# Kernel optimization log

Hardware: AMD Instinct MI355X
Metric: run time of the kernel (lower is better)

## Reference

```python
import jax, jax.numpy as jnp
import numpy as np

T, B, F_, H, D, C = 16, 1024, 512, 128, 8, 100  # trees, batch, feat, hidden, depth, classes
L = 2 ** (D + 1)  # n_leaf = 512


def _routing_tables():
    # Static per-leaf routing: node index and branch side at each depth.
    # Derived from compute_mu's gather indices:
    #   node(d, l) = 2^d - 1 + l // 2^(D+1-d);  side(d, l) = (l // 2^(D-d)) % 2
    l = np.arange(L)
    node = np.stack([(2 ** d - 1) + l // (2 ** (D + 1 - d)) for d in range(D + 1)])  # [D+1, L]
    side = np.stack([(l // (2 ** (D - d))) % 2 for d in range(D + 1)])               # [D+1, L]
    return jnp.asarray(node, dtype=jnp.int32), jnp.asarray(side.astype(np.bool_))


def setup_inputs() -> dict:
    key = jax.random.key(0)
    ks = jax.random.split(key, 4)
    return {
        "feat": jax.random.normal(ks[0], (B, F_), jnp.float32),
        "W1": jax.random.normal(ks[1], (T, F_, H), jnp.float32) * 0.05,
        "b1": jnp.zeros((T, H), jnp.float32),
        "W2": jax.random.normal(ks[2], (T, H, L), jnp.float32) * 0.05,
        "b2": jnp.zeros((T, L), jnp.float32),
        "pi": jax.random.uniform(ks[3], (T, L, C), jnp.float32, -2.0, 2.0),
    }


def reference(feat, W1, b1, W2, b2, pi):
    node, side = _routing_tables()
    # Per-tree MLP head (dropout is identity in eval mode).
    h = jax.nn.relu(jnp.einsum('bf,tfh->tbh', feat, W1) + b1[:, None, :])        # [T,B,H]
    p = jax.nn.sigmoid(jnp.einsum('tbh,thl->tbl', h, W2) + b2[:, None, :])       # [T,B,L]
    # compute_mu: product of routing probs along each root->leaf path.
    sel = p[:, :, node]                          # [T,B,D+1,L] gather (static indices)
    route = jnp.where(side, 1.0 - sel, sel)      # left -> p, right -> 1-p
    mu = jnp.prod(route, axis=2)                 # [T,B,L]
    # compute_py_x: mean over leaves then mean over trees of mu @ softmax(pi).
    leaf_p = jax.nn.softmax(pi, axis=-1)         # [T,L,C]
    py_x = jnp.einsum('tbl,tlc->bc', mu, leaf_p) / (L * T)  # [B,C]
    return jnp.log(py_x)
```

## Files before the change

kernel.cpp:

```cpp
#include <hip/hip_runtime.h>
#include <hip/hip_bf16.h>
#include <math.h>

#define T_ 16
#define B_ 1024
#define F_ 512
#define H_ 128
#define D_ 8
#define C_ 100
#define L_ 512
#define CP_ 112

typedef __attribute__((ext_vector_type(8))) short bf16x8_t;
typedef __attribute__((ext_vector_type(4))) float f32x4_t;

__device__ inline ushort f2bf(float x) {
  __hip_bfloat16 b = __float2bfloat16(x);
  return *(ushort*)&b;
}
__device__ inline float bf2f(ushort u) {
  union { unsigned int i; float f; } v;
  v.i = ((unsigned int)u) << 16;
  return v.f;
}

__global__ __launch_bounds__(256) void k_prep(
    const float* __restrict__ feat, const float* __restrict__ W1,
    const float* __restrict__ W2, const float* __restrict__ pi,
    ushort* __restrict__ feat_bf, ushort* __restrict__ W1T,
    ushort* __restrict__ W2T, ushort* __restrict__ lpT) {
  __shared__ ushort ubuf[112 * 48];
  float (*tile)[33] = (float(*)[33])ubuf;
  ushort (*tileT)[48] = (ushort(*)[48])ubuf;
  const int bid = blockIdx.x, tid = threadIdx.x;

  if (bid < 256) {
    int i = (bid * 256 + tid) * 8;
    float4 a = *(const float4*)(feat + i);
    float4 b = *(const float4*)(feat + i + 4);
    bf16x8_t o;
    o[0] = (short)f2bf(a.x); o[1] = (short)f2bf(a.y);
    o[2] = (short)f2bf(a.z); o[3] = (short)f2bf(a.w);
    o[4] = (short)f2bf(b.x); o[5] = (short)f2bf(b.y);
    o[6] = (short)f2bf(b.z); o[7] = (short)f2bf(b.w);
    *(bf16x8_t*)(feat_bf + i) = o;
    return;
  }
  if (bid < 2304) {
    const float* X; ushort* XT; int K, N, kb, nb, s;
    if (bid < 1280) {
      int r = bid - 256;  kb = r & 15; nb = (r >> 4) & 3;  s = r >> 6;
      X = W1; XT = W1T; K = F_; N = H_;
    } else {
      int r = bid - 1280; kb = r & 3;  nb = (r >> 2) & 15; s = r >> 6;
      X = W2; XT = W2T; K = H_; N = L_;
    }
    const int k0 = kb * 32, n0 = nb * 32;
    const int c = tid & 31, r0 = tid >> 5;
    const float* Xs = X + (size_t)s * K * N;
    ushort* XTs = XT + (size_t)s * N * K;
#pragma unroll
    for (int j = 0; j < 4; ++j)
      tile[r0 + 8 * j][c] = Xs[(size_t)(k0 + r0 + 8 * j) * N + n0 + c];
    __syncthreads();
#pragma unroll
    for (int j = 0; j < 4; ++j)
      XTs[(size_t)(n0 + r0 + 8 * j) * K + k0 + c] = f2bf(tile[c][r0 + 8 * j]);
    return;
  }
  {
    int bid2 = bid - 2304;
    int t = bid2 >> 4, l0 = (bid2 & 15) << 5;
    int lane = tid & 63;
#pragma unroll
    for (int p = 0; p < 8; ++p) {
      int rl = p * 4 + (tid >> 6);
      const float* x = pi + (size_t)(t * L_ + l0 + rl) * C_;
      float v0 = (lane < C_) ? x[lane] : -1e30f;
      float v1 = (lane + 64 < C_) ? x[lane + 64] : -1e30f;
      float m = fmaxf(v0, v1);
#pragma unroll
      for (int off = 32; off; off >>= 1) m = fmaxf(m, __shfl_xor(m, off, 64));
      float e0 = __expf(v0 - m);
      float e1 = (lane + 64 < C_) ? __expf(v1 - m) : 0.0f;
      float sm = e0 + e1;
#pragma unroll
      for (int off = 32; off; off >>= 1) sm += __shfl_xor(sm, off, 64);
      float inv = 1.0f / sm;
      if (lane < C_) tileT[lane][rl] = f2bf(e0 * inv);
      int c2 = lane + 64;
      if (c2 < CP_) tileT[c2][rl] = f2bf(c2 < C_ ? e1 * inv : 0.0f);
    }
    __syncthreads();
    ushort* dst = lpT + (size_t)t * CP_ * L_ + l0;
    for (int idx = tid; idx < 448; idx += 256) {
      int c = idx >> 2, ch = (idx & 3) * 8;
      *(bf16x8_t*)(dst + (size_t)c * L_ + ch) = *(const bf16x8_t*)&tileT[c][ch];
    }
  }
}

__global__ __launch_bounds__(256) void k12_mfma(
    const ushort* __restrict__ feat, const ushort* __restrict__ W1T,
    const float* __restrict__ b1, const ushort* __restrict__ W2T,
    const float* __restrict__ b2, const ushort* __restrict__ lpT,
    float* __restrict__ part) {
  __shared__ ushort smem[29696];
  ushort (*h_s)[136] = (ushort(*)[136])smem;
  ushort (*a_s)[72]  = (ushort(*)[72])(smem + 4352);
  ushort (*b_s)[72]  = (ushort(*)[72])(smem + 6656);
  ushort (*w_s)[136] = (ushort(*)[136])(smem + 4352);
  ushort (*p_s)[520] = (ushort(*)[520])(smem + 13056);

  const int bid = blockIdx.x;
  const int t = bid & 15, b0 = (bid >> 4) * 32;
  const int tid = threadIdx.x;
  const int w = tid >> 6, lane = tid & 63, quad = lane >> 4, n = lane & 15;

  const int arow = tid >> 3, acol = (tid & 7) * 8;
  const ushort* featp = feat + (size_t)(b0 + arow) * F_ + acol;
  const ushort* w1p   = W1T + ((size_t)t * H_ + arow) * F_ + acol;

  {
    f32x4_t acc[2][2];
#pragma unroll
    for (int i = 0; i < 2; ++i)
#pragma unroll
      for (int j = 0; j < 2; ++j) acc[i][j] = (f32x4_t){0.f, 0.f, 0.f, 0.f};

    bf16x8_t ra, rb[4];
    ra = *(const bf16x8_t*)(featp);
#pragma unroll
    for (int i = 0; i < 4; ++i)
      rb[i] = *(const bf16x8_t*)(w1p + (size_t)i * 32 * F_);
    *(bf16x8_t*)&a_s[arow][acol] = ra;
#pragma unroll
    for (int i = 0; i < 4; ++i)
      *(bf16x8_t*)&b_s[i * 32 + arow][acol] = rb[i];
    __syncthreads();
    ra = *(const bf16x8_t*)(featp + 64);
#pragma unroll
    for (int i = 0; i < 4; ++i)
      rb[i] = *(const bf16x8_t*)(w1p + (size_t)i * 32 * F_ + 64);

#pragma unroll
    for (int kc = 0; kc < 8; ++kc) {
#pragma unroll
      for (int ks = 0; ks < 64; ks += 32) {
        bf16x8_t af[2], bfr[2];
#pragma unroll
        for (int mt = 0; mt < 2; ++mt)
          af[mt] = *(const bf16x8_t*)&a_s[mt * 16 + n][ks + quad * 8];
#pragma unroll
        for (int nt = 0; nt < 2; ++nt)
          bfr[nt] = *(const bf16x8_t*)&b_s[w * 32 + nt * 16 + n][ks + quad * 8];
#pragma unroll
        for (int mt = 0; mt < 2; ++mt)
#pragma unroll
          for (int nt = 0; nt < 2; ++nt)
            acc[mt][nt] = __builtin_amdgcn_mfma_f32_16x16x32_bf16(
                af[mt], bfr[nt], acc[mt][nt], 0, 0, 0);
      }
      __syncthreads();
      if (kc < 7) {
        *(bf16x8_t*)&a_s[arow][acol] = ra;
#pragma unroll
        for (int i = 0; i < 4; ++i)
          *(bf16x8_t*)&b_s[i * 32 + arow][acol] = rb[i];
        __syncthreads();
        if (kc < 6) {
          ra = *(const bf16x8_t*)(featp + (kc + 2) * 64);
#pragma unroll
          for (int i = 0; i < 4; ++i)
            rb[i] = *(const bf16x8_t*)(w1p + (size_t)i * 32 * F_ + (kc + 2) * 64);
        }
      }
    }
    float bias[2] = {b1[t * H_ + w * 32 + n], b1[t * H_ + w * 32 + 16 + n]};
#pragma unroll
    for (int mt = 0; mt < 2; ++mt)
#pragma unroll
      for (int nt = 0; nt < 2; ++nt)
#pragma unroll
        for (int r = 0; r < 4; ++r) {
          int row = mt * 16 + quad * 4 + r;
          int col = w * 32 + nt * 16 + n;
          float v = acc[mt][nt][r] + bias[nt];
          h_s[row][col] = f2bf(v > 0.f ? v : 0.f);
        }
  }

  {
    const int wrow = tid >> 4, wcol = (tid & 15) * 8;
    const ushort* w2p = W2T + ((size_t)t * L_ + wrow) * H_ + wcol;
    bf16x8_t rw[4];
#pragma unroll
    for (int i = 0; i < 4; ++i)
      rw[i] = *(const bf16x8_t*)(w2p + (size_t)(i * 16) * H_);
    __syncthreads();

    bf16x8_t af2[2][4];
#pragma unroll
    for (int mt = 0; mt < 2; ++mt)
#pragma unroll
      for (int ks = 0; ks < 4; ++ks)
        af2[mt][ks] = *(const bf16x8_t*)&h_s[mt * 16 + n][ks * 32 + quad * 8];
#pragma unroll
    for (int i = 0; i < 4; ++i)
      *(bf16x8_t*)&w_s[i * 16 + wrow][wcol] = rw[i];
    __syncthreads();
#pragma unroll
    for (int i = 0; i < 4; ++i)
      rw[i] = *(const bf16x8_t*)(w2p + (size_t)(64 + i * 16) * H_);

#pragma unroll
    for (int nc = 0; nc < 8; ++nc) {
      f32x4_t acc[2];
      acc[0] = (f32x4_t){0.f, 0.f, 0.f, 0.f};
      acc[1] = (f32x4_t){0.f, 0.f, 0.f, 0.f};
#pragma unroll
      for (int ks = 0; ks < 4; ++ks) {
        bf16x8_t bfrag = *(const bf16x8_t*)&w_s[w * 16 + n][ks * 32 + quad * 8];
        acc[0] = __builtin_amdgcn_mfma_f32_16x16x32_bf16(af2[0][ks], bfrag,
                                                         acc[0], 0, 0, 0);
        acc[1] = __builtin_amdgcn_mfma_f32_16x16x32_bf16(af2[1][ks], bfrag,
                                                         acc[1], 0, 0, 0);
      }
      int l = nc * 64 + w * 16 + n;
      float bias = b2[t * L_ + l];
#pragma unroll
      for (int mt = 0; mt < 2; ++mt)
#pragma unroll
        for (int r = 0; r < 4; ++r) {
          float x = acc[mt][r] + bias;
          p_s[mt * 16 + quad * 4 + r][l] = f2bf(1.0f / (1.0f + __expf(-x)));
        }
      __syncthreads();
      if (nc < 7) {
#pragma unroll
        for (int i = 0; i < 4; ++i)
          *(bf16x8_t*)&w_s[i * 16 + wrow][wcol] = rw[i];
        __syncthreads();
        if (nc < 6) {
#pragma unroll
          for (int i = 0; i < 4; ++i)
            rw[i] = *(const bf16x8_t*)(w2p + (size_t)((nc + 2) * 64 + i * 16) * H_);
        }
      }
    }
  }
  __syncthreads();

  bf16x8_t mo[4][2];
#pragma unroll
  for (int pass = 0; pass < 4; ++pass) {
    int b = pass * 8 + (tid >> 5);
    int s = tid & 31;
    float P = 1.f;
#pragma unroll
    for (int d = 0; d < 5; ++d) {
      int nd = (1 << d) - 1 + (s >> (5 - d));
      int sd = (s >> (4 - d)) & 1;
      float pv = bf2f(p_s[b][nd]);
      P *= sd ? (1.f - pv) : pv;
    }
    float p5 = bf2f(p_s[b][31 + s]);
    float q5[2] = {P * p5, P * (1.f - p5)};
    float q6[4], q7[8];
#pragma unroll
    for (int j = 0; j < 2; ++j) {
      float pv = bf2f(p_s[b][63 + 2 * s + j]);
      q6[2 * j] = q5[j] * pv;
      q6[2 * j + 1] = q5[j] * (1.f - pv);
    }
#pragma unroll
    for (int u = 0; u < 4; ++u) {
      float pv = bf2f(p_s[b][127 + 4 * s + u]);
      q7[2 * u] = q6[u] * pv;
      q7[2 * u + 1] = q6[u] * (1.f - pv);
    }
    bf16x8_t o0, o1;
#pragma unroll
    for (int v = 0; v < 8; ++v) {
      float pv = bf2f(p_s[b][255 + 8 * s + v]);
      ushort e0 = f2bf(q7[v] * pv);
      ushort e1 = f2bf(q7[v] * (1.f - pv));
      if (v < 4) { o0[2 * v] = (short)e0; o0[2 * v + 1] = (short)e1; }
      else       { o1[2 * (v - 4)] = (short)e0; o1[2 * (v - 4) + 1] = (short)e1; }
    }
    mo[pass][0] = o0;
    mo[pass][1] = o1;
  }
  __syncthreads();
#pragma unroll
  for (int pass = 0; pass < 4; ++pass) {
    int b = pass * 8 + (tid >> 5);
    int s = tid & 31;
    *(bf16x8_t*)&p_s[b][s * 16]     = mo[pass][0];
    *(bf16x8_t*)&p_s[b][s * 16 + 8] = mo[pass][1];
  }
  __syncthreads();

  {
    const int mt = w >> 1;
    const int nt0 = (w & 1) * 4;
    const int ncnt = (w & 1) ? 3 : 4;
    const ushort* arow2 = &p_s[mt * 16 + n][0];
    const ushort* brow = lpT + (size_t)t * CP_ * L_ +
                         ((size_t)(nt0 * 16 + n)) * L_ + quad * 8;
    f32x4_t acc[4];
#pragma unroll
    for (int i = 0; i < 4; ++i) acc[i] = (f32x4_t){0.f, 0.f, 0.f, 0.f};
#pragma unroll 4
    for (int k = 0; k < L_; k += 32) {
      bf16x8_t af = *(const bf16x8_t*)(arow2 + k + quad * 8);
#pragma unroll
      for (int j = 0; j < 4; ++j) {
        if (j < ncnt) {
          bf16x8_t bfr = *(const bf16x8_t*)(brow + (size_t)j * 16 * L_ + k);
          acc[j] = __builtin_amdgcn_mfma_f32_16x16x32_bf16(af, bfr, acc[j],
                                                           0, 0, 0);
        }
      }
    }
    const int m0 = b0 + mt * 16 + quad * 4;
#pragma unroll
    for (int j = 0; j < 4; ++j) {
      int c = (nt0 + j) * 16 + n;
      if (j < ncnt && c < C_) {
#pragma unroll
        for (int r = 0; r < 4; ++r)
          part[((size_t)t * B_ + m0 + r) * C_ + c] = acc[j][r];
      }
    }
  }
}

__global__ __launch_bounds__(256) void k6_log(
    const float* __restrict__ part, float* __restrict__ out) {
  int i = blockIdx.x * 256 + threadIdx.x;
  if (i < B_ * C_) {
    float s = 0.0f;
#pragma unroll
    for (int t = 0; t < T_; ++t) s += part[(size_t)t * B_ * C_ + i];
    out[i] = logf(s * (1.0f / (L_ * T_)));
  }
}

extern "C" void kernel_launch(void* const* d_in, const int* in_sizes, int n_in,
                              void* d_out, int out_size, void* d_ws,
                              size_t ws_size, hipStream_t stream) {
  const float* feat = (const float*)d_in[0];
  const float* W1   = (const float*)d_in[1];
  const float* b1   = (const float*)d_in[2];
  const float* W2   = (const float*)d_in[3];
  const float* b2   = (const float*)d_in[4];
  const float* pi   = (const float*)d_in[5];
  float* out = (float*)d_out;

  char* ws = (char*)d_ws;
  ushort* feat_bf  = (ushort*)(ws);
  ushort* W1T_buf  = (ushort*)(ws + ((size_t)1 << 20));
  ushort* W2T_buf  = (ushort*)(ws + ((size_t)3 << 20));
  ushort* lpT_buf  = (ushort*)(ws + ((size_t)5 << 20));
  float*  part_buf = (float*)(ws + ((size_t)7 << 20));

  k_prep<<<2560, 256, 0, stream>>>(feat, W1, W2, pi, feat_bf, W1T_buf,
                                   W2T_buf, lpT_buf);
  k12_mfma<<<512, 256, 0, stream>>>(feat_bf, W1T_buf, b1, W2T_buf, b2,
                                    lpT_buf, part_buf);
  k6_log<<<(B_ * C_ + 255) / 256, 256, 0, stream>>>(part_buf, out);
}
```

Baseline: 110.5 us.

## Deepen global prefetch to two stages and relax barriers in fused MLP kernel

The fused MLP kernel now holds two register buffers of global prefetch for both GEMM phases, loading two K-chunks ahead instead of one. Plain __syncthreads are replaced with raw s_barrier calls, some of which skip the lgkmcnt wait, so outstanding global loads are not drained at each barrier. The final log-reduction kernel is also vectorized to float4 loads and stores. This should hide more global latency, at the cost of more registers and some risk from the hand-written barrier semantics.

```diff
diff --git a/kernel.cpp b/kernel.cpp
--- a/kernel.cpp
+++ b/kernel.cpp
@@ -22,6 +22,17 @@
   union { unsigned int i; float f; } v;
   v.i = ((unsigned int)u) << 16;
   return v.f;
+}
+
+__device__ inline void bar_raw() {
+  asm volatile("" ::: "memory");
+  __builtin_amdgcn_s_barrier();
+  asm volatile("" ::: "memory");
+}
+__device__ inline void bar_publish_lds() {
+  asm volatile("s_waitcnt lgkmcnt(0)" ::: "memory");
+  __builtin_amdgcn_s_barrier();
+  asm volatile("" ::: "memory");
 }
 
 __global__ __launch_bounds__(256) void k_prep(
@@ -128,20 +139,24 @@
 #pragma unroll
       for (int j = 0; j < 2; ++j) acc[i][j] = (f32x4_t){0.f, 0.f, 0.f, 0.f};
 
-    bf16x8_t ra, rb[4];
-    ra = *(const bf16x8_t*)(featp);
-#pragma unroll
-    for (int i = 0; i < 4; ++i)
-      rb[i] = *(const bf16x8_t*)(w1p + (size_t)i * 32 * F_);
-    *(bf16x8_t*)&a_s[arow][acol] = ra;
-#pragma unroll
-    for (int i = 0; i < 4; ++i)
-      *(bf16x8_t*)&b_s[i * 32 + arow][acol] = rb[i];
-    __syncthreads();
-    ra = *(const bf16x8_t*)(featp + 64);
-#pragma unroll
-    for (int i = 0; i < 4; ++i)
-      rb[i] = *(const bf16x8_t*)(w1p + (size_t)i * 32 * F_ + 64);
+    bf16x8_t ra[2], rb[2][4];
+    ra[0] = *(const bf16x8_t*)(featp);
+#pragma unroll
+    for (int i = 0; i < 4; ++i)
+      rb[0][i] = *(const bf16x8_t*)(w1p + (size_t)i * 32 * F_);
+    *(bf16x8_t*)&a_s[arow][acol] = ra[0];
+#pragma unroll
+    for (int i = 0; i < 4; ++i)
+      *(bf16x8_t*)&b_s[i * 32 + arow][acol] = rb[0][i];
+    bar_publish_lds();
+    ra[1] = *(const bf16x8_t*)(featp + 64);
+#pragma unroll
+    for (int i = 0; i < 4; ++i)
+      rb[1][i] = *(const bf16x8_t*)(w1p + (size_t)i * 32 * F_ + 64);
+    ra[0] = *(const bf16x8_t*)(featp + 128);
+#pragma unroll
+    for (int i = 0; i < 4; ++i)
+      rb[0][i] = *(const bf16x8_t*)(w1p + (size_t)i * 32 * F_ + 128);
 
 #pragma unroll
     for (int kc = 0; kc < 8; ++kc) {
@@ -161,18 +176,19 @@
             acc[mt][nt] = __builtin_amdgcn_mfma_f32_16x16x32_bf16(
                 af[mt], bfr[nt], acc[mt][nt], 0, 0, 0);
       }
-      __syncthreads();
+      bar_raw();
       if (kc < 7) {
-        *(bf16x8_t*)&a_s[arow][acol] = ra;
+        const int p = (kc + 1) & 1;
+        *(bf16x8_t*)&a_s[arow][acol] = ra[p];
 #pragma unroll
         for (int i = 0; i < 4; ++i)
-          *(bf16x8_t*)&b_s[i * 32 + arow][acol] = rb[i];
-        __syncthreads();
+          *(bf16x8_t*)&b_s[i * 32 + arow][acol] = rb[p][i];
+        bar_publish_lds();
         if (kc < 6) {
-          ra = *(const bf16x8_t*)(featp + (kc + 2) * 64);
+          ra[p] = *(const bf16x8_t*)(featp + (kc + 3) * 64);
 #pragma unroll
           for (int i = 0; i < 4; ++i)
-            rb[i] = *(const bf16x8_t*)(w1p + (size_t)i * 32 * F_ + (kc + 2) * 64);
+            rb[p][i] = *(const bf16x8_t*)(w1p + (size_t)i * 32 * F_ + (kc + 3) * 64);
         }
       }
     }
@@ -193,11 +209,14 @@
   {
     const int wrow = tid >> 4, wcol = (tid & 15) * 8;
     const ushort* w2p = W2T + ((size_t)t * L_ + wrow) * H_ + wcol;
-    bf16x8_t rw[4];
-#pragma unroll
-    for (int i = 0; i < 4; ++i)
-      rw[i] = *(const bf16x8_t*)(w2p + (size_t)(i * 16) * H_);
-    __syncthreads();
+    bf16x8_t rw[2][4];
+#pragma unroll
+    for (int i = 0; i < 4; ++i)
+      rw[0][i] = *(const bf16x8_t*)(w2p + (size_t)(i * 16) * H_);
+#pragma unroll
+    for (int i = 0; i < 4; ++i)
+      rw[1][i] = *(const bf16x8_t*)(w2p + (size_t)(64 + i * 16) * H_);
+    bar_publish_lds();
 
     bf16x8_t af2[2][4];
 #pragma unroll
@@ -207,11 +226,11 @@
         af2[mt][ks] = *(const bf16x8_t*)&h_s[mt * 16 + n][ks * 32 + quad * 8];
 #pragma unroll
     for (int i = 0; i < 4; ++i)
-      *(bf16x8_t*)&w_s[i * 16 + wrow][wcol] = rw[i];
-    __syncthreads();
-#pragma unroll
-    for (int i = 0; i < 4; ++i)
-      rw[i] = *(const bf16x8_t*)(w2p + (size_t)(64 + i * 16) * H_);
+      *(bf16x8_t*)&w_s[i * 16 + wrow][wcol] = rw[0][i];
+    bar_publish_lds();
+#pragma unroll
+    for (int i = 0; i < 4; ++i)
+      rw[0][i] = *(const bf16x8_t*)(w2p + (size_t)(128 + i * 16) * H_);
 
 #pragma unroll
     for (int nc = 0; nc < 8; ++nc) {
@@ -235,21 +254,22 @@
           float x = acc[mt][r] + bias;
           p_s[mt * 16 + quad * 4 + r][l] = f2bf(1.0f / (1.0f + __expf(-x)));
         }
-      __syncthreads();
+      bar_raw();
       if (nc < 7) {
+        const int p = (nc + 1) & 1;
 #pragma unroll
         for (int i = 0; i < 4; ++i)
-          *(bf16x8_t*)&w_s[i * 16 + wrow][wcol] = rw[i];
-        __syncthreads();
+          *(bf16x8_t*)&w_s[i * 16 + wrow][wcol] = rw[p][i];
+        bar_publish_lds();
         if (nc < 6) {
 #pragma unroll
           for (int i = 0; i < 4; ++i)
-            rw[i] = *(const bf16x8_t*)(w2p + (size_t)((nc + 2) * 64 + i * 16) * H_);
+            rw[p][i] = *(const bf16x8_t*)(w2p + (size_t)((nc + 3) * 64 + i * 16) * H_);
         }
       }
     }
   }
-  __syncthreads();
+  bar_publish_lds();
 
   bf16x8_t mo[4][2];
 #pragma unroll
@@ -291,7 +311,7 @@
     mo[pass][0] = o0;
     mo[pass][1] = o1;
   }
-  __syncthreads();
+  bar_raw();
 #pragma unroll
   for (int pass = 0; pass < 4; ++pass) {
     int b = pass * 8 + (tid >> 5);
@@ -299,7 +319,7 @@
     *(bf16x8_t*)&p_s[b][s * 16]     = mo[pass][0];
     *(bf16x8_t*)&p_s[b][s * 16 + 8] = mo[pass][1];
   }
-  __syncthreads();
+  bar_publish_lds();
 
   {
     const int mt = w >> 1;
@@ -338,12 +358,19 @@
 
 __global__ __launch_bounds__(256) void k6_log(
     const float* __restrict__ part, float* __restrict__ out) {
-  int i = blockIdx.x * 256 + threadIdx.x;
+  int i = (blockIdx.x * 256 + threadIdx.x) * 4;
   if (i < B_ * C_) {
-    float s = 0.0f;
-#pragma unroll
-    for (int t = 0; t < T_; ++t) s += part[(size_t)t * B_ * C_ + i];
-    out[i] = logf(s * (1.0f / (L_ * T_)));
+    float4 s = {0.f, 0.f, 0.f, 0.f};
+#pragma unroll
+    for (int t = 0; t < T_; ++t) {
+      float4 v = *(const float4*)(part + (size_t)t * B_ * C_ + i);
+      s.x += v.x; s.y += v.y; s.z += v.z; s.w += v.w;
+    }
+    const float inv = 1.0f / (L_ * T_);
+    float4 o;
+    o.x = logf(s.x * inv); o.y = logf(s.y * inv);
+    o.z = logf(s.z * inv); o.w = logf(s.w * inv);
+    *(float4*)(out + i) = o;
   }
 }
 
@@ -369,5 +396,5 @@
                                    W2T_buf, lpT_buf);
   k12_mfma<<<512, 256, 0, stream>>>(feat_bf, W1T_buf, b1, W2T_buf, b2,
                                     lpT_buf, part_buf);
-  k6_log<<<(B_ * C_ + 255) / 256, 256, 0, stream>>>(part_buf, out);
-}
+  k6_log<<<(B_ * C_ / 4 + 255) / 256, 256, 0, stream>>>(part_buf, out);
+}
```

Result: no change. 109.0 us (-1.4%).
